# Kernel tuning notes

Hardware: AMD Instinct MI355X
Metric: run time of the kernel (lower is better)

The kernel has to match this reference:

```python
import jax, jax.numpy as jnp
import numpy as np

EPS = 1e-12  # F.normalize eps


def _l2norm(v, axis):
    n = jnp.sqrt(jnp.sum(v * v, axis=axis, keepdims=True))
    return v / jnp.maximum(n, EPS)


def setup_inputs() -> dict:
    key = jax.random.key(0)
    k1, k2, k3, k4 = jax.random.split(key, 4)
    N, C, H, W = 48, 512, 40, 40
    K = 64
    x = jax.random.normal(k1, (N, C, H, W), dtype=jnp.float32)
    conv_w = jax.random.normal(k2, (K, C), dtype=jnp.float32) * 0.02   # cluster-assign 1x1 conv, no bias (vladv2=False)
    attn_w = jax.random.normal(k3, (1, C), dtype=jnp.float32) * 0.02   # heatmap 1x1 conv
    attn_b = jnp.zeros((1,), dtype=jnp.float32)
    centroids = jax.random.uniform(k4, (K, C), dtype=jnp.float32)      # torch.rand init
    return {"x": x, "conv_w": conv_w, "attn_w": attn_w, "attn_b": attn_b, "centroids": centroids}


def reference(x, conv_w, attn_w, attn_b, centroids):
    N, C, H, W = x.shape
    K = conv_w.shape[0]
    P = H * W

    # attention heatmap: ReLU -> 1x1 conv -> ReLU  => [N, 1, H, W]
    hmp = jax.nn.relu(jnp.einsum('nchw,oc->nohw', jax.nn.relu(x), attn_w) + attn_b[None, :, None, None])
    hmp_flat = hmp.reshape(N, 1, P)  # [N,1,P]

    # normalize input descriptors across channels
    xn = _l2norm(x, axis=1)                      # [N,C,H,W]
    x_flat = xn.reshape(N, C, P)                 # [N,C,P]

    # soft assignment: 1x1 conv over clusters + softmax over cluster dim
    logits = jnp.einsum('ncp,kc->nkp', x_flat, conv_w)   # [N,K,P]
    soft_assign = jax.nn.softmax(logits, axis=1)          # softmax over K

    # weighted residual aggregation, fused:
    # vlad[n,k,c] = sum_p (x[n,c,p] - centroids[k,c]) * sa[n,k,p] * hmp[n,0,p]
    w = soft_assign * hmp_flat                            # [N,K,P]
    term1 = jnp.einsum('nkp,ncp->nkc', w, x_flat)         # [N,K,C]
    wsum = jnp.sum(w, axis=-1)                            # [N,K]
    vlad = term1 - wsum[:, :, None] * centroids[None, :, :]

    vlad = _l2norm(vlad, axis=2)                          # intra-normalize per cluster
    vlad = vlad.reshape(N, K * C)
    vlad = _l2norm(vlad, axis=1)                          # global L2 normalize
    return vlad
```

## Files before the change

kernel.cpp:

```cpp
#include <hip/hip_runtime.h>
#include <math.h>

#define NN 48
#define CC 512
#define KK 64
#define PP 1600
#define EPSF 1e-12f

typedef short short8 __attribute__((ext_vector_type(8)));
typedef float f32x4 __attribute__((ext_vector_type(4)));

static __device__ __forceinline__ unsigned short f2bf(float f) {
    unsigned u = __float_as_uint(f);
    u += 0x7fffu + ((u >> 16) & 1u);
    return (unsigned short)(u >> 16);
}
static __device__ __forceinline__ unsigned pack2(float a, float b) {
    return (unsigned)f2bf(a) | ((unsigned)f2bf(b) << 16);
}

__global__ __launch_bounds__(256) void kn_logits(
    const float* __restrict__ x, const float* __restrict__ conv_w,
    const float* __restrict__ attn_w, const float* __restrict__ attn_b,
    unsigned short* __restrict__ wg, float* __restrict__ wsum,
    unsigned short* __restrict__ xbf)
{
    __shared__ unsigned short xt[64][140];
    __shared__ unsigned short cwb[64][72];
    __shared__ float attn_l[CC];
    __shared__ float red[8][128];
    __shared__ float invn_l[128];
    __shared__ float hmp_l[128];

    const int n = blockIdx.y, p0 = blockIdx.x * 128, tid = threadIdx.x;
    const int q = tid & 31, cg8 = tid >> 5;
    const int wave = tid >> 6, lane = tid & 63;
    const int lq = lane >> 4, lm = lane & 15;
    const bool pval = (p0 + q * 4) < PP;

    for (int i = tid; i < CC; i += 256) attn_l[i] = attn_w[i];

    f32x4 acc[4][2];
#pragma unroll
    for (int mt = 0; mt < 4; ++mt)
#pragma unroll
        for (int nt = 0; nt < 2; ++nt) acc[mt][nt] = (f32x4){0.f, 0.f, 0.f, 0.f};
    float ss[4] = {0.f, 0.f, 0.f, 0.f};
    float ad[4] = {0.f, 0.f, 0.f, 0.f};

    const float* xb = x + (size_t)n * CC * PP;
    __syncthreads();

    for (int cs = 0; cs < 8; ++cs) {
        const int c0 = cs * 64;
        {
            const int kr = tid >> 2, cq = tid & 3;
            const float* wp = conv_w + kr * CC + c0 + cq * 16;
#pragma unroll
            for (int j = 0; j < 4; ++j) {
                float4 v = *(const float4*)(wp + 4 * j);
                uint2 u = {pack2(v.x, v.y), pack2(v.z, v.w)};
                *(uint2*)&cwb[kr][cq * 16 + 4 * j] = u;
            }
        }
#pragma unroll
        for (int j = 0; j < 8; ++j) {
            const int cl = cg8 * 8 + j, cg = c0 + cl;
            float4 v = make_float4(0.f, 0.f, 0.f, 0.f);
            if (pval) v = *(const float4*)(xb + (size_t)cg * PP + p0 + 4 * q);
            const float aw = attn_l[cg];
            ss[0] += v.x * v.x; ss[1] += v.y * v.y;
            ss[2] += v.z * v.z; ss[3] += v.w * v.w;
            ad[0] += fmaxf(v.x, 0.f) * aw; ad[1] += fmaxf(v.y, 0.f) * aw;
            ad[2] += fmaxf(v.z, 0.f) * aw; ad[3] += fmaxf(v.w, 0.f) * aw;
            uint2 u = {pack2(v.x, v.y), pack2(v.z, v.w)};
            *(uint2*)&xt[cl][4 * q] = u;
            if (xbf && pval)
                *(uint2*)(xbf + ((size_t)n * CC + cg) * PP + p0 + 4 * q) = u;
        }
        __syncthreads();
#pragma unroll
        for (int ks = 0; ks < 2; ++ks) {
            short8 af[4];
#pragma unroll
            for (int mt = 0; mt < 4; ++mt)
                af[mt] = *(const short8*)&cwb[mt * 16 + lm][ks * 32 + lq * 8];
#pragma unroll
            for (int nt = 0; nt < 2; ++nt) {
                const int pl = wave * 32 + nt * 16 + lm;
                const int cb = ks * 32 + lq * 8;
                short8 bv;
#pragma unroll
                for (int j = 0; j < 8; ++j) bv[j] = (short)xt[cb + j][pl];
#pragma unroll
                for (int mt = 0; mt < 4; ++mt)
                    acc[mt][nt] = __builtin_amdgcn_mfma_f32_16x16x32_bf16(
                        af[mt], bv, acc[mt][nt], 0, 0, 0);
            }
        }
        __syncthreads();
    }

#pragma unroll
    for (int j = 0; j < 4; ++j) red[cg8][q * 4 + j] = ss[j];
    __syncthreads();
    if (tid < 128) {
        float S = 0.f;
#pragma unroll
        for (int l = 0; l < 8; ++l) S += red[l][tid];
        invn_l[tid] = 1.f / fmaxf(sqrtf(S), EPSF);
    }
    __syncthreads();
#pragma unroll
    for (int j = 0; j < 4; ++j) red[cg8][q * 4 + j] = ad[j];
    __syncthreads();
    if (tid < 128) {
        float A = 0.f;
#pragma unroll
        for (int l = 0; l < 8; ++l) A += red[l][tid];
        hmp_l[tid] = fmaxf(A + attn_b[0], 0.f);
    }
    __syncthreads();

    float invv[2], sden[2];
#pragma unroll
    for (int nt = 0; nt < 2; ++nt) {
        const int pl = wave * 32 + nt * 16 + lm;
        const bool pv = (p0 + pl) < PP;
        const float inv = invn_l[pl];
        const float hp = pv ? hmp_l[pl] : 0.f;
        float mx = -1e30f;
#pragma unroll
        for (int mt = 0; mt < 4; ++mt)
#pragma unroll
            for (int r = 0; r < 4; ++r) {
                const float l = acc[mt][nt][r] * inv;
                acc[mt][nt][r] = l;
                mx = fmaxf(mx, l);
            }
        mx = fmaxf(mx, __shfl_xor(mx, 16));
        mx = fmaxf(mx, __shfl_xor(mx, 32));
        float s = 0.f;
#pragma unroll
        for (int mt = 0; mt < 4; ++mt)
#pragma unroll
            for (int r = 0; r < 4; ++r) {
                const float e = __expf(acc[mt][nt][r] - mx);
                acc[mt][nt][r] = e;
                s += e;
            }
        s += __shfl_xor(s, 16);
        s += __shfl_xor(s, 32);
        sden[nt] = hp / s;
        invv[nt] = inv;
    }

    const int pl0 = wave * 32 + lm, pl1 = pl0 + 16;
    const bool v0 = (p0 + pl0) < PP, v1 = (p0 + pl1) < PP;
#pragma unroll
    for (int mt = 0; mt < 4; ++mt)
#pragma unroll
        for (int r = 0; r < 4; ++r) {
            const int k = mt * 16 + lq * 4 + r;
            const float w0 = acc[mt][0][r] * sden[0];
            const float w1 = acc[mt][1][r] * sden[1];
            float wk = w0 + w1;
#pragma unroll
            for (int o = 1; o < 16; o <<= 1) wk += __shfl_xor(wk, o);
            if (lm == 0) atomicAdd(&wsum[n * KK + k], wk);
            unsigned short* wr = wg + ((size_t)n * KK + k) * PP + p0;
            if (v0) wr[pl0] = f2bf(w0 * invv[0]);
            if (v1) wr[pl1] = f2bf(w1 * invv[1]);
        }
}

template <bool XB>
__global__ __launch_bounds__(256) void kn_term1(
    const float* __restrict__ xf, const unsigned short* __restrict__ xbf,
    const unsigned short* __restrict__ wgq, float* __restrict__ term1p)
{
    __shared__ unsigned short wt[64][40];
    __shared__ unsigned short xt2[128][40];
    const int c0 = blockIdx.x * 128, n = blockIdx.y, ph = blockIdx.z;
    const int tid = threadIdx.x;
    const int wave = tid >> 6, lane = tid & 63, lq = lane >> 4, lm = lane & 15;
    const int koff = (wave >> 1) * 32, coff = (wave & 1) * 64;
    const int s_begin = (50 * ph) >> 2, s_end = (50 * (ph + 1)) >> 2;

    const int rA = tid >> 2, cqA = tid & 3;
    const int rB0 = tid >> 2, cqB0 = tid & 3;
    const int rB1 = (256 + tid) >> 2, cqB1 = tid & 3;

    f32x4 acc[2][4];
#pragma unroll
    for (int mt = 0; mt < 2; ++mt)
#pragma unroll
        for (int nt = 0; nt < 4; ++nt) acc[mt][nt] = (f32x4){0.f, 0.f, 0.f, 0.f};

    const unsigned short* wb = wgq + (size_t)n * KK * PP;

    auto ldA = [&](int p0) -> uint4 {
        return *(const uint4*)(wb + (size_t)rA * PP + p0 + cqA * 8);
    };
    auto ldB = [&](int p0, int row, int cq) -> uint4 {
        if (XB) {
            return *(const uint4*)(xbf + ((size_t)n * CC + c0 + row) * PP + p0 + cq * 8);
        } else {
            const float* sp = xf + ((size_t)n * CC + c0 + row) * PP + p0 + cq * 8;
            float4 a = *(const float4*)sp, b = *(const float4*)(sp + 4);
            return make_uint4(pack2(a.x, a.y), pack2(a.z, a.w),
                              pack2(b.x, b.y), pack2(b.z, b.w));
        }
    };

    uint4 pa = ldA(s_begin * 32);
    uint4 pb0 = ldB(s_begin * 32, rB0, cqB0);
    uint4 pb1 = ldB(s_begin * 32, rB1, cqB1);

    for (int ps = s_begin; ps < s_end; ++ps) {
        *(uint4*)&wt[rA][cqA * 8] = pa;
        *(uint4*)&xt2[rB0][cqB0 * 8] = pb0;
        *(uint4*)&xt2[rB1][cqB1 * 8] = pb1;
        __syncthreads();
        uint4 na, nb0, nb1;
        if (ps + 1 < s_end) {
            const int p1 = (ps + 1) * 32;
            na = ldA(p1); nb0 = ldB(p1, rB0, cqB0); nb1 = ldB(p1, rB1, cqB1);
        }
        short8 af[2], bv[4];
#pragma unroll
        for (int mt = 0; mt < 2; ++mt)
            af[mt] = *(const short8*)&wt[koff + mt * 16 + lm][lq * 8];
#pragma unroll
        for (int nt = 0; nt < 4; ++nt)
            bv[nt] = *(const short8*)&xt2[coff + nt * 16 + lm][lq * 8];
#pragma unroll
        for (int mt = 0; mt < 2; ++mt)
#pragma unroll
            for (int nt = 0; nt < 4; ++nt)
                acc[mt][nt] = __builtin_amdgcn_mfma_f32_16x16x32_bf16(
                    af[mt], bv[nt], acc[mt][nt], 0, 0, 0);
        __syncthreads();
        pa = na; pb0 = nb0; pb1 = nb1;
    }

    float* ob = term1p + ((size_t)ph * NN + n) * KK * CC;
#pragma unroll
    for (int mt = 0; mt < 2; ++mt)
#pragma unroll
        for (int r = 0; r < 4; ++r) {
            const int k = koff + mt * 16 + lq * 4 + r;
#pragma unroll
            for (int nt = 0; nt < 4; ++nt)
                ob[(size_t)k * CC + c0 + coff + nt * 16 + lm] = acc[mt][nt][r];
        }
}

__global__ __launch_bounds__(128) void kn_vlad(
    const float* __restrict__ term1p, const float* __restrict__ wsum,
    const float* __restrict__ cent, float* __restrict__ out,
    float* __restrict__ nsum)
{
    const int k = blockIdx.x, n = blockIdx.y, tid = threadIdx.x;
    const size_t base = ((size_t)n * KK + k) * CC;
    const size_t NKC = (size_t)NN * KK * CC;
    const float ws = wsum[n * KK + k];
    const int c = tid * 4;

    float4 ce = *(const float4*)(cent + (size_t)k * CC + c);
    float4 v = {-ws * ce.x, -ws * ce.y, -ws * ce.z, -ws * ce.w};
#pragma unroll
    for (int h = 0; h < 4; ++h) {
        float4 a = *(const float4*)(term1p + h * NKC + base + c);
        v.x += a.x; v.y += a.y; v.z += a.z; v.w += a.w;
    }

    float s = v.x * v.x + v.y * v.y + v.z * v.z + v.w * v.w;
#pragma unroll
    for (int o = 32; o >= 1; o >>= 1) s += __shfl_down(s, o, 64);

    __shared__ float rb[2];
    __shared__ float sinv;
    if ((tid & 63) == 0) rb[tid >> 6] = s;
    __syncthreads();
    if (tid == 0) {
        const float S = rb[0] + rb[1];
        const float inv = 1.f / fmaxf(sqrtf(S), EPSF);
        sinv = inv;
        atomicAdd(&nsum[n], S * inv * inv);
    }
    __syncthreads();
    const float inv = sinv;
    float4 o4 = {v.x * inv, v.y * inv, v.z * inv, v.w * inv};
    *(float4*)(out + base + c) = o4;
}

__global__ __launch_bounds__(256) void kn_scale(
    float* __restrict__ out, const float* __restrict__ nsum)
{
    const int n = blockIdx.y;
    const size_t off = ((size_t)blockIdx.x * 256 + threadIdx.x) * 4;
    const float g = 1.f / fmaxf(sqrtf(nsum[n]), EPSF);
    float4 v = *(float4*)(out + (size_t)n * KK * CC + off);
    v.x *= g; v.y *= g; v.z *= g; v.w *= g;
    *(float4*)(out + (size_t)n * KK * CC + off) = v;
}

extern "C" void kernel_launch(void* const* d_in, const int* in_sizes, int n_in,
                              void* d_out, int out_size, void* d_ws, size_t ws_size,
                              hipStream_t stream)
{
    (void)in_sizes; (void)n_in; (void)out_size;
    const float* x      = (const float*)d_in[0];
    const float* conv_w = (const float*)d_in[1];
    const float* attn_w = (const float*)d_in[2];
    const float* attn_b = (const float*)d_in[3];
    const float* cent   = (const float*)d_in[4];
    float* out = (float*)d_out;

    char* w = (char*)d_ws;
    float* term1p = (float*)w;            w += (size_t)4 * NN * KK * CC * 4;
    float* wsum   = (float*)w;            w += (size_t)NN * KK * 4;
    float* nsum   = (float*)w;            w += 256;
    unsigned short* wg  = (unsigned short*)w; w += (size_t)NN * KK * PP * 2;
    unsigned short* xbf = (unsigned short*)w;
    const size_t need_xb = (size_t)(w - (char*)d_ws) + (size_t)NN * CC * PP * 2;
    const bool xb = ws_size >= need_xb;

    hipMemsetAsync(wsum, 0, NN * KK * sizeof(float), stream);
    hipMemsetAsync(nsum, 0, NN * sizeof(float), stream);

    kn_logits<<<dim3(13, NN), 256, 0, stream>>>(x, conv_w, attn_w, attn_b,
                                                wg, wsum, xb ? xbf : nullptr);
    if (xb)
        kn_term1<true><<<dim3(4, NN, 4), 256, 0, stream>>>(x, xbf, wg, term1p);
    else
        kn_term1<false><<<dim3(4, NN, 4), 256, 0, stream>>>(x, xbf, wg, term1p);
    kn_vlad <<<dim3(KK, NN), 128, 0, stream>>>(term1p, wsum, cent, out, nsum);
    kn_scale<<<dim3(32, NN), 256, 0, stream>>>(out, nsum);
}
```

Baseline: 315.2 us.

## Shrink logits/term1 tiles, prefetch next chunk in registers, aggregate wsum in LDS

The logits kernel now handles 64 pixels per block instead of 128, which doubles the grid (25x48 blocks) and removes the ragged-tail bounds checks, since 1600 divides evenly by 64. It also prefetches the next channel chunk of x and conv_w into registers while the current chunk is processed. Per-cluster wsum partials are first accumulated in shared memory, so each block issues one global atomic per cluster instead of one per wave. The term1 kernel uses 64-channel tiles, doubling its grid, with one load per thread per stage. The aim is more parallelism and occupancy and better latency hiding, at the cost of more blocks and more redundant conv_w loads.

```diff
diff --git a/kernel.cpp b/kernel.cpp
--- a/kernel.cpp
+++ b/kernel.cpp
@@ -19,64 +19,76 @@
     return (unsigned)f2bf(a) | ((unsigned)f2bf(b) << 16);
 }
 
-__global__ __launch_bounds__(256) void kn_logits(
+__global__ __launch_bounds__(256, 4) void kn_logits(
     const float* __restrict__ x, const float* __restrict__ conv_w,
     const float* __restrict__ attn_w, const float* __restrict__ attn_b,
     unsigned short* __restrict__ wg, float* __restrict__ wsum,
     unsigned short* __restrict__ xbf)
 {
-    __shared__ unsigned short xt[64][140];
+    __shared__ unsigned short xt[64][76];
     __shared__ unsigned short cwb[64][72];
     __shared__ float attn_l[CC];
-    __shared__ float red[8][128];
-    __shared__ float invn_l[128];
-    __shared__ float hmp_l[128];
-
-    const int n = blockIdx.y, p0 = blockIdx.x * 128, tid = threadIdx.x;
-    const int q = tid & 31, cg8 = tid >> 5;
+    __shared__ float red[16][64];
+    __shared__ float invn_l[64];
+    __shared__ float hmp_l[64];
+    __shared__ float wsum_l[KK];
+
+    const int n = blockIdx.y, p0 = blockIdx.x * 64, tid = threadIdx.x;
+    const int q = tid & 15, cg = tid >> 4;
     const int wave = tid >> 6, lane = tid & 63;
     const int lq = lane >> 4, lm = lane & 15;
-    const bool pval = (p0 + q * 4) < PP;
+    const int kr = tid >> 2, cq = tid & 3;
 
     for (int i = tid; i < CC; i += 256) attn_l[i] = attn_w[i];
-
-    f32x4 acc[4][2];
-#pragma unroll
-    for (int mt = 0; mt < 4; ++mt)
-#pragma unroll
-        for (int nt = 0; nt < 2; ++nt) acc[mt][nt] = (f32x4){0.f, 0.f, 0.f, 0.f};
+    if (tid < KK) wsum_l[tid] = 0.f;
+
+    f32x4 acc[4];
+#pragma unroll
+    for (int mt = 0; mt < 4; ++mt) acc[mt] = (f32x4){0.f, 0.f, 0.f, 0.f};
     float ss[4] = {0.f, 0.f, 0.f, 0.f};
     float ad[4] = {0.f, 0.f, 0.f, 0.f};
 
     const float* xb = x + (size_t)n * CC * PP;
-    __syncthreads();
-
+    const float* wp0 = conv_w + (size_t)kr * CC + cq * 16;
+    const float* xp0 = xb + (size_t)(cg * 4) * PP + p0 + 4 * q;
+
+    float4 wv[4], xv[4];
+#pragma unroll
+    for (int j = 0; j < 4; ++j) wv[j] = *(const float4*)(wp0 + 4 * j);
+#pragma unroll
+    for (int j = 0; j < 4; ++j) xv[j] = *(const float4*)(xp0 + (size_t)j * PP);
+
+    __syncthreads();
+
+#pragma unroll 1
     for (int cs = 0; cs < 8; ++cs) {
-        const int c0 = cs * 64;
-        {
-            const int kr = tid >> 2, cq = tid & 3;
-            const float* wp = conv_w + kr * CC + c0 + cq * 16;
-#pragma unroll
-            for (int j = 0; j < 4; ++j) {
-                float4 v = *(const float4*)(wp + 4 * j);
-                uint2 u = {pack2(v.x, v.y), pack2(v.z, v.w)};
-                *(uint2*)&cwb[kr][cq * 16 + 4 * j] = u;
-            }
-        }
-#pragma unroll
-        for (int j = 0; j < 8; ++j) {
-            const int cl = cg8 * 8 + j, cg = c0 + cl;
-            float4 v = make_float4(0.f, 0.f, 0.f, 0.f);
-            if (pval) v = *(const float4*)(xb + (size_t)cg * PP + p0 + 4 * q);
-            const float aw = attn_l[cg];
+        float4 wn[4], xn_[4];
+        if (cs < 7) {
+            const float* wp = wp0 + (cs + 1) * 64;
+            const float* xp = xp0 + (size_t)(cs + 1) * 64 * PP;
+#pragma unroll
+            for (int j = 0; j < 4; ++j) wn[j] = *(const float4*)(wp + 4 * j);
+#pragma unroll
+            for (int j = 0; j < 4; ++j) xn_[j] = *(const float4*)(xp + (size_t)j * PP);
+        }
+#pragma unroll
+        for (int j = 0; j < 4; ++j) {
+            uint2 u = {pack2(wv[j].x, wv[j].y), pack2(wv[j].z, wv[j].w)};
+            *(uint2*)&cwb[kr][cq * 16 + 4 * j] = u;
+        }
+        const int cbase = cs * 64 + cg * 4;
+#pragma unroll
+        for (int j = 0; j < 4; ++j) {
+            float4 v = xv[j];
+            const float aw = attn_l[cbase + j];
             ss[0] += v.x * v.x; ss[1] += v.y * v.y;
             ss[2] += v.z * v.z; ss[3] += v.w * v.w;
             ad[0] += fmaxf(v.x, 0.f) * aw; ad[1] += fmaxf(v.y, 0.f) * aw;
             ad[2] += fmaxf(v.z, 0.f) * aw; ad[3] += fmaxf(v.w, 0.f) * aw;
             uint2 u = {pack2(v.x, v.y), pack2(v.z, v.w)};
-            *(uint2*)&xt[cl][4 * q] = u;
-            if (xbf && pval)
-                *(uint2*)(xbf + ((size_t)n * CC + cg) * PP + p0 + 4 * q) = u;
+            *(uint2*)&xt[cg * 4 + j][4 * q] = u;
+            if (xbf)
+                *(uint2*)(xbf + ((size_t)n * CC + cbase + j) * PP + p0 + 4 * q) = u;
         }
         __syncthreads();
 #pragma unroll
@@ -85,93 +97,86 @@
 #pragma unroll
             for (int mt = 0; mt < 4; ++mt)
                 af[mt] = *(const short8*)&cwb[mt * 16 + lm][ks * 32 + lq * 8];
-#pragma unroll
-            for (int nt = 0; nt < 2; ++nt) {
-                const int pl = wave * 32 + nt * 16 + lm;
-                const int cb = ks * 32 + lq * 8;
-                short8 bv;
-#pragma unroll
-                for (int j = 0; j < 8; ++j) bv[j] = (short)xt[cb + j][pl];
-#pragma unroll
-                for (int mt = 0; mt < 4; ++mt)
-                    acc[mt][nt] = __builtin_amdgcn_mfma_f32_16x16x32_bf16(
-                        af[mt], bv, acc[mt][nt], 0, 0, 0);
-            }
+            const int pl = wave * 16 + lm;
+            const int cb = ks * 32 + lq * 8;
+            short8 bv;
+#pragma unroll
+            for (int j = 0; j < 8; ++j) bv[j] = (short)xt[cb + j][pl];
+#pragma unroll
+            for (int mt = 0; mt < 4; ++mt)
+                acc[mt] = __builtin_amdgcn_mfma_f32_16x16x32_bf16(
+                    af[mt], bv, acc[mt], 0, 0, 0);
         }
         __syncthreads();
-    }
-
-#pragma unroll
-    for (int j = 0; j < 4; ++j) red[cg8][q * 4 + j] = ss[j];
-    __syncthreads();
-    if (tid < 128) {
+        if (cs < 7) {
+#pragma unroll
+            for (int j = 0; j < 4; ++j) { wv[j] = wn[j]; xv[j] = xn_[j]; }
+        }
+    }
+
+#pragma unroll
+    for (int j = 0; j < 4; ++j) red[cg][4 * q + j] = ss[j];
+    __syncthreads();
+    if (tid < 64) {
         float S = 0.f;
 #pragma unroll
-        for (int l = 0; l < 8; ++l) S += red[l][tid];
+        for (int l = 0; l < 16; ++l) S += red[l][tid];
         invn_l[tid] = 1.f / fmaxf(sqrtf(S), EPSF);
     }
     __syncthreads();
 #pragma unroll
-    for (int j = 0; j < 4; ++j) red[cg8][q * 4 + j] = ad[j];
-    __syncthreads();
-    if (tid < 128) {
+    for (int j = 0; j < 4; ++j) red[cg][4 * q + j] = ad[j];
+    __syncthreads();
+    if (tid < 64) {
         float A = 0.f;
 #pragma unroll
-        for (int l = 0; l < 8; ++l) A += red[l][tid];
+        for (int l = 0; l < 16; ++l) A += red[l][tid];
         hmp_l[tid] = fmaxf(A + attn_b[0], 0.f);
     }
     __syncthreads();
 
-    float invv[2], sden[2];
-#pragma unroll
-    for (int nt = 0; nt < 2; ++nt) {
-        const int pl = wave * 32 + nt * 16 + lm;
-        const bool pv = (p0 + pl) < PP;
-        const float inv = invn_l[pl];
-        const float hp = pv ? hmp_l[pl] : 0.f;
-        float mx = -1e30f;
-#pragma unroll
-        for (int mt = 0; mt < 4; ++mt)
-#pragma unroll
-            for (int r = 0; r < 4; ++r) {
-                const float l = acc[mt][nt][r] * inv;
-                acc[mt][nt][r] = l;
-                mx = fmaxf(mx, l);
-            }
-        mx = fmaxf(mx, __shfl_xor(mx, 16));
-        mx = fmaxf(mx, __shfl_xor(mx, 32));
-        float s = 0.f;
-#pragma unroll
-        for (int mt = 0; mt < 4; ++mt)
-#pragma unroll
-            for (int r = 0; r < 4; ++r) {
-                const float e = __expf(acc[mt][nt][r] - mx);
-                acc[mt][nt][r] = e;
-                s += e;
-            }
-        s += __shfl_xor(s, 16);
-        s += __shfl_xor(s, 32);
-        sden[nt] = hp / s;
-        invv[nt] = inv;
-    }
-
-    const int pl0 = wave * 32 + lm, pl1 = pl0 + 16;
-    const bool v0 = (p0 + pl0) < PP, v1 = (p0 + pl1) < PP;
+    const int pl = wave * 16 + lm;
+    const float inv = invn_l[pl];
+    const float hp = hmp_l[pl];
+    float mx = -1e30f;
+#pragma unroll
+    for (int mt = 0; mt < 4; ++mt)
+#pragma unroll
+        for (int r = 0; r < 4; ++r) {
+            const float l = acc[mt][r] * inv;
+            acc[mt][r] = l;
+            mx = fmaxf(mx, l);
+        }
+    mx = fmaxf(mx, __shfl_xor(mx, 16));
+    mx = fmaxf(mx, __shfl_xor(mx, 32));
+    float s = 0.f;
+#pragma unroll
+    for (int mt = 0; mt < 4; ++mt)
+#pragma unroll
+        for (int r = 0; r < 4; ++r) {
+            const float e = __expf(acc[mt][r] - mx);
+            acc[mt][r] = e;
+            s += e;
+        }
+    s += __shfl_xor(s, 16);
+    s += __shfl_xor(s, 32);
+    const float sden = hp / s;
+
+    unsigned short* wrb = wg + (size_t)n * KK * PP + p0;
 #pragma unroll
     for (int mt = 0; mt < 4; ++mt)
 #pragma unroll
         for (int r = 0; r < 4; ++r) {
             const int k = mt * 16 + lq * 4 + r;
-            const float w0 = acc[mt][0][r] * sden[0];
-            const float w1 = acc[mt][1][r] * sden[1];
-            float wk = w0 + w1;
+            const float w0 = acc[mt][r] * sden;
+            float wk = w0;
 #pragma unroll
             for (int o = 1; o < 16; o <<= 1) wk += __shfl_xor(wk, o);
-            if (lm == 0) atomicAdd(&wsum[n * KK + k], wk);
-            unsigned short* wr = wg + ((size_t)n * KK + k) * PP + p0;
-            if (v0) wr[pl0] = f2bf(w0 * invv[0]);
-            if (v1) wr[pl1] = f2bf(w1 * invv[1]);
-        }
+            if (lm == 0) atomicAdd(&wsum_l[k], wk);
+            wrb[(size_t)k * PP + pl] = f2bf(w0 * inv);
+        }
+    __syncthreads();
+    if (tid < KK) atomicAdd(&wsum[n * KK + tid], wsum_l[tid]);
 }
 
 template <bool XB>
@@ -180,79 +185,71 @@
     const unsigned short* __restrict__ wgq, float* __restrict__ term1p)
 {
     __shared__ unsigned short wt[64][40];
-    __shared__ unsigned short xt2[128][40];
-    const int c0 = blockIdx.x * 128, n = blockIdx.y, ph = blockIdx.z;
+    __shared__ unsigned short xt2[64][40];
+    const int c0 = blockIdx.x * 64, n = blockIdx.y, ph = blockIdx.z;
     const int tid = threadIdx.x;
     const int wave = tid >> 6, lane = tid & 63, lq = lane >> 4, lm = lane & 15;
-    const int koff = (wave >> 1) * 32, coff = (wave & 1) * 64;
+    const int koff = (wave >> 1) * 32, coff = (wave & 1) * 32;
     const int s_begin = (50 * ph) >> 2, s_end = (50 * (ph + 1)) >> 2;
-
-    const int rA = tid >> 2, cqA = tid & 3;
-    const int rB0 = tid >> 2, cqB0 = tid & 3;
-    const int rB1 = (256 + tid) >> 2, cqB1 = tid & 3;
-
-    f32x4 acc[2][4];
+    const int rA = tid >> 2, cq = tid & 3;
+
+    f32x4 acc[2][2];
 #pragma unroll
     for (int mt = 0; mt < 2; ++mt)
 #pragma unroll
-        for (int nt = 0; nt < 4; ++nt) acc[mt][nt] = (f32x4){0.f, 0.f, 0.f, 0.f};
-
-    const unsigned short* wb = wgq + (size_t)n * KK * PP;
-
-    auto ldA = [&](int p0) -> uint4 {
-        return *(const uint4*)(wb + (size_t)rA * PP + p0 + cqA * 8);
-    };
-    auto ldB = [&](int p0, int row, int cq) -> uint4 {
+        for (int nt = 0; nt < 2; ++nt) acc[mt][nt] = (f32x4){0.f, 0.f, 0.f, 0.f};
+
+    const unsigned short* wb = wgq + (size_t)n * KK * PP + (size_t)rA * PP + cq * 8;
+    const unsigned short* xbb = xbf + ((size_t)n * CC + c0 + rA) * PP + cq * 8;
+    const float* xfb = xf + ((size_t)n * CC + c0 + rA) * PP + cq * 8;
+
+    auto ldB = [&](int p) -> uint4 {
         if (XB) {
-            return *(const uint4*)(xbf + ((size_t)n * CC + c0 + row) * PP + p0 + cq * 8);
+            return *(const uint4*)(xbb + p);
         } else {
-            const float* sp = xf + ((size_t)n * CC + c0 + row) * PP + p0 + cq * 8;
+            const float* sp = xfb + p;
             float4 a = *(const float4*)sp, b = *(const float4*)(sp + 4);
             return make_uint4(pack2(a.x, a.y), pack2(a.z, a.w),
                               pack2(b.x, b.y), pack2(b.z, b.w));
         }
     };
 
-    uint4 pa = ldA(s_begin * 32);
-    uint4 pb0 = ldB(s_begin * 32, rB0, cqB0);
-    uint4 pb1 = ldB(s_begin * 32, rB1, cqB1);
+    uint4 pa = *(const uint4*)(wb + s_begin * 32);
+    uint4 pb = ldB(s_begin * 32);
 
     for (int ps = s_begin; ps < s_end; ++ps) {
-        *(uint4*)&wt[rA][cqA * 8] = pa;
-        *(uint4*)&xt2[rB0][cqB0 * 8] = pb0;
-        *(uint4*)&xt2[rB1][cqB1 * 8] = pb1;
+        *(uint4*)&wt[rA][cq * 8] = pa;
+        *(uint4*)&xt2[rA][cq * 8] = pb;
         __syncthreads();
-        uint4 na, nb0, nb1;
         if (ps + 1 < s_end) {
-            const int p1 = (ps + 1) * 32;
-            na = ldA(p1); nb0 = ldB(p1, rB0, cqB0); nb1 = ldB(p1, rB1, cqB1);
-        }
-        short8 af[2], bv[4];
+            pa = *(const uint4*)(wb + (ps + 1) * 32);
+            pb = ldB((ps + 1) * 32);
+        }
+        short8 af[2], bv[2];
 #pragma unroll
         for (int mt = 0; mt < 2; ++mt)
             af[mt] = *(const short8*)&wt[koff + mt * 16 + lm][lq * 8];
 #pragma unroll
-        for (int nt = 0; nt < 4; ++nt)
+        for (int nt = 0; nt < 2; ++nt)
             bv[nt] = *(const short8*)&xt2[coff + nt * 16 + lm][lq * 8];
 #pragma unroll
         for (int mt = 0; mt < 2; ++mt)
 #pragma unroll
-            for (int nt = 0; nt < 4; ++nt)
+            for (int nt = 0; nt < 2; ++nt)
                 acc[mt][nt] = __builtin_amdgcn_mfma_f32_16x16x32_bf16(
                     af[mt], bv[nt], acc[mt][nt], 0, 0, 0);
         __syncthreads();
-        pa = na; pb0 = nb0; pb1 = nb1;
-    }
-
-    float* ob = term1p + ((size_t)ph * NN + n) * KK * CC;
+    }
+
+    float* ob = term1p + ((size_t)ph * NN + n) * KK * CC + c0 + coff;
 #pragma unroll
     for (int mt = 0; mt < 2; ++mt)
 #pragma unroll
         for (int r = 0; r < 4; ++r) {
             const int k = koff + mt * 16 + lq * 4 + r;
 #pragma unroll
-            for (int nt = 0; nt < 4; ++nt)
-                ob[(size_t)k * CC + c0 + coff + nt * 16 + lm] = acc[mt][nt][r];
+            for (int nt = 0; nt < 2; ++nt)
+                ob[(size_t)k * CC + nt * 16 + lm] = acc[mt][nt][r];
         }
 }
 
@@ -330,12 +327,12 @@
     hipMemsetAsync(wsum, 0, NN * KK * sizeof(float), stream);
     hipMemsetAsync(nsum, 0, NN * sizeof(float), stream);
 
-    kn_logits<<<dim3(13, NN), 256, 0, stream>>>(x, conv_w, attn_w, attn_b,
+    kn_logits<<<dim3(25, NN), 256, 0, stream>>>(x, conv_w, attn_w, attn_b,
                                                 wg, wsum, xb ? xbf : nullptr);
     if (xb)
-        kn_term1<true><<<dim3(4, NN, 4), 256, 0, stream>>>(x, xbf, wg, term1p);
+        kn_term1<true><<<dim3(8, NN, 4), 256, 0, stream>>>(x, xbf, wg, term1p);
     else
-        kn_term1<false><<<dim3(4, NN, 4), 256, 0, stream>>>(x, xbf, wg, term1p);
+        kn_term1<false><<<dim3(8, NN, 4), 256, 0, stream>>>(x, xbf, wg, term1p);
     kn_vlad <<<dim3(KK, NN), 128, 0, stream>>>(term1p, wsum, cent, out, nsum);
     kn_scale<<<dim3(32, NN), 256, 0, stream>>>(out, nsum);
 }
```

Result: slower. 322.2 us (+2.2%).
